# Kernel tuning notes

Measured on AMD Instinct MI355X. Metric: run time of the kernel, lower is better.

The kernel has to match this reference:

```python
import jax, jax.numpy as jnp
import numpy as np
from jax import lax

B, C, H, W, D = 2, 64, 32, 32, 32
N = H * W * D          # input_size = 32768
P = 64                 # proj_size
NH = 4                 # num_heads
HD = C // NH           # head dim = 16
LN_EPS = 1e-5
BN_EPS = 1e-5


def setup_inputs() -> dict:
    key = jax.random.key(0)
    ks = jax.random.split(key, 10)
    s = lambda k, shape: (jax.random.normal(k, shape, jnp.float32) * 0.02)
    return dict(
        x=jax.random.normal(ks[0], (B, C, H, W, D), jnp.float32),
        ln_w=jnp.ones((C,), jnp.float32), ln_b=jnp.zeros((C,), jnp.float32),
        gamma=1e-6 * jnp.ones((C,), jnp.float32),
        temp1=jnp.ones((NH, 1, 1), jnp.float32),
        temp2=jnp.ones((NH, 1, 1), jnp.float32),
        W_qkvv=s(ks[1], (4 * C, C)),                      # Linear(C,4C), no bias
        W_EF=s(ks[2], (P, N)), b_EF=jnp.zeros((P,), jnp.float32),  # shared E=F
        W_o1=s(ks[3], (C // 2, C)), b_o1=jnp.zeros((C // 2,), jnp.float32),
        W_o2=s(ks[4], (C // 2, C)), b_o2=jnp.zeros((C // 2,), jnp.float32),
        conv1_w=s(ks[5], (C, C, 3, 3, 3)),
        conv2_w=s(ks[6], (C, C, 3, 3, 3)),
        bn1_w=jnp.ones((C,), jnp.float32), bn1_b=jnp.zeros((C,), jnp.float32),
        bn2_w=jnp.ones((C,), jnp.float32), bn2_b=jnp.zeros((C,), jnp.float32),
        conv8_w=s(ks[7], (C, C, 1, 1, 1)), conv8_b=jnp.zeros((C,), jnp.float32),
    )


def _ln(x, w, b):
    mu = jnp.mean(x, axis=-1, keepdims=True)
    var = jnp.mean(jnp.square(x - mu), axis=-1, keepdims=True)
    return (x - mu) * lax.rsqrt(var + LN_EPS) * w + b


def _l2norm(x):  # F.normalize(dim=-1), eps=1e-12
    n = jnp.sqrt(jnp.sum(jnp.square(x), axis=-1, keepdims=True))
    return x / jnp.maximum(n, 1e-12)


def _bn_eval(x, w, b):  # BatchNorm3d in eval mode, running mean 0 / var 1
    scale = (w * lax.rsqrt(jnp.float32(1.0 + BN_EPS))).reshape(1, -1, 1, 1, 1)
    return x * scale + b.reshape(1, -1, 1, 1, 1)


def _conv3d(x, w, pad):
    return lax.conv_general_dilated(
        x, w, window_strides=(1, 1, 1), padding=[(pad, pad)] * 3,
        dimension_numbers=('NCDHW', 'OIDHW', 'NCDHW'))


def _lrelu(x):
    return jnp.where(x >= 0, x, 0.01 * x)


def _epa(xn, W_qkvv, W_EF, b_EF, temp1, temp2, W_o1, b_o1, W_o2, b_o2):
    b, n, c = xn.shape
    qkvv = (xn @ W_qkvv.T).reshape(b, n, 4, NH, HD).transpose(2, 0, 3, 1, 4)  # [4,B,h,N,d]
    q, k, v_ca, v_sa = [jnp.swapaxes(qkvv[i], -2, -1) for i in range(4)]      # [B,h,d,N]
    # shared linear projection E = F over the token axis N -> P
    k_proj = jnp.einsum('bhdn,pn->bhdp', k, W_EF) + b_EF
    v_proj = jnp.einsum('bhdn,pn->bhdp', v_sa, W_EF) + b_EF
    qn, kn = _l2norm(q), _l2norm(k)
    # channel attention: [B,h,d,d]
    attn_ca = jax.nn.softmax(jnp.einsum('bhdn,bhen->bhde', qn, kn) * temp1, axis=-1)
    x_ca = jnp.einsum('bhde,bhen->bhdn', attn_ca, v_ca)                       # [B,h,d,N]
    x_ca = x_ca.transpose(0, 3, 1, 2).reshape(b, n, c)
    # spatial attention with projected K/V: [B,h,N,P]
    attn_sa = jax.nn.softmax(jnp.einsum('bhdn,bhdp->bhnp', qn, k_proj) * temp2, axis=-1)
    x_sa = jnp.einsum('bhnp,bhdp->bhnd', attn_sa, v_proj)                     # [B,h,N,d]
    # faithful to original UNETR++ code: permute(0,3,1,2) then reshape(B,N,C)
    x_sa = x_sa.transpose(0, 3, 1, 2).reshape(b, n, c)
    x_sa = x_sa @ W_o1.T + b_o1
    x_ca = x_ca @ W_o2.T + b_o2
    return jnp.concatenate([x_sa, x_ca], axis=-1)


def reference(x, ln_w, ln_b, gamma, temp1, temp2, W_qkvv, W_EF, b_EF,
              W_o1, b_o1, W_o2, b_o2, conv1_w, conv2_w,
              bn1_w, bn1_b, bn2_w, bn2_b, conv8_w, conv8_b):
    b, c, h, w, d = x.shape
    xs = x.reshape(b, c, h * w * d).transpose(0, 2, 1)  # [B,N,C]
    attn = xs + gamma * _epa(_ln(xs, ln_w, ln_b), W_qkvv, W_EF, b_EF,
                             temp1, temp2, W_o1, b_o1, W_o2, b_o2)
    attn_skip = attn.reshape(b, h, w, d, c).transpose(0, 4, 1, 2, 3)  # [B,C,H,W,D]
    # UnetResBlock (stride 1, in==out -> identity residual), BN in eval mode
    out = _lrelu(_bn_eval(_conv3d(attn_skip, conv1_w, 1), bn1_w, bn1_b))
    out = _bn_eval(_conv3d(out, conv2_w, 1), bn2_w, bn2_b)
    out = _lrelu(out + attn_skip)
    # conv8: Dropout3d (off, eval) + 1x1x1 conv with bias
    y = _conv3d(out, conv8_w, 0) + conv8_b.reshape(1, -1, 1, 1, 1)
    return attn_skip + y
```

## Files before the change

kernel.cpp:

```cpp
#include <hip/hip_runtime.h>

#define NTOK 32768

typedef __attribute__((ext_vector_type(8))) short short8;
typedef __attribute__((ext_vector_type(4))) short short4_t;
typedef __attribute__((ext_vector_type(4))) float f32x4;

__device__ __forceinline__ short f2b(float f) {
    union { float f; unsigned u; } v; v.f = f;
    unsigned r = v.u + 0x7fffu + ((v.u >> 16) & 1u);
    return (short)(r >> 16);
}
__device__ __forceinline__ float b2f(short s) {
    union { float f; unsigned u; } v;
    v.u = ((unsigned)(unsigned short)s) << 16;
    return v.f;
}

__global__ void k_repack(const float* __restrict__ w1, const float* __restrict__ w2,
                         const float* __restrict__ w8, const float* __restrict__ wef,
                         const float* __restrict__ wq, const float* __restrict__ bEF,
                         short* __restrict__ wb1, short* __restrict__ wb2,
                         short* __restrict__ wb8, short* __restrict__ wefb,
                         short* __restrict__ wqb, float* __restrict__ kp,
                         float* __restrict__ vp, float* __restrict__ qd)
{
    int i = blockIdx.x * 256 + threadIdx.x;
    if (i >= 2349312) return;
    if (i >= 2347008) { qd[i - 2347008] = 0.f; return; }
    if (i >= 2338816) {
        int j = i - 2338816;
        float v = bEF[j & 63];
        kp[j] = v; vp[j] = v; return;
    }
    if (i >= 2322432) { int j = i - 2322432; wqb[j] = f2b(wq[j]); return; }
    if (i >= 225280)  { int j = i - 225280;  wefb[j] = f2b(wef[j]); return; }
    if (i >= 221184)  { int j = i - 221184;  wb8[j] = f2b(w8[j]); return; }
    int sel = i >= 110592;
    int j = sel ? i - 110592 : i;
    int tap = j >> 12;
    int r = j & 4095;
    int oc = r >> 6, ic = r & 63;
    const float* w = sel ? w2 : w1;
    short* o = sel ? wb2 : wb1;
    o[j] = f2b(w[(oc * 64 + ic) * 27 + tap]);
}

__global__ __launch_bounds__(256) void k_ln_qkvv(
    const float* __restrict__ x, const float* __restrict__ lnw,
    const float* __restrict__ lnb, const short* __restrict__ wqb,
    short* __restrict__ qkvvb)
{
    __shared__ __align__(16) short Wl[256 * 72];
    __shared__ __align__(16) short tr[256 * 72];
    __shared__ float red1[4][64], red2[4][64];
    __shared__ float mu_s[64], rs_s[64];
    short* al = tr;

    int bid = blockIdx.x;
    int b = bid >> 9;
    int n0 = (bid & 511) << 6;
    int tid = threadIdx.x;

    for (int i = tid; i < 2048; i += 256) {
        int out = i >> 3, q8 = (i & 7) * 8;
        *(short8*)&Wl[out * 72 + q8] = *(const short8*)&wqb[out * 64 + q8];
    }

    int t = tid & 63, cq = tid >> 6;
    float xr[16];
    float s1 = 0.f, s2 = 0.f;
    const float* xb = x + (((size_t)(b * 64 + cq * 16)) << 15) + n0 + t;
#pragma unroll
    for (int j = 0; j < 16; ++j) {
        float v = xb[(size_t)j << 15];
        xr[j] = v; s1 += v; s2 += v * v;
    }
    red1[cq][t] = s1; red2[cq][t] = s2;
    __syncthreads();
    if (tid < 64) {
        float a = red1[0][tid] + red1[1][tid] + red1[2][tid] + red1[3][tid];
        float q = red2[0][tid] + red2[1][tid] + red2[2][tid] + red2[3][tid];
        float mu = a * (1.f / 64.f);
        float var = q * (1.f / 64.f) - mu * mu;
        mu_s[tid] = mu;
        rs_s[tid] = rsqrtf(var + 1e-5f);
    }
    __syncthreads();
    {
        float mu = mu_s[t], rs = rs_s[t];
        short8 p0, p1;
#pragma unroll
        for (int j = 0; j < 8; ++j) {
            int c = cq * 16 + j;
            p0[j] = f2b((xr[j] - mu) * rs * lnw[c] + lnb[c]);
        }
#pragma unroll
        for (int j = 0; j < 8; ++j) {
            int c = cq * 16 + 8 + j;
            p1[j] = f2b((xr[8 + j] - mu) * rs * lnw[c] + lnb[c]);
        }
        *(short8*)&al[t * 72 + cq * 16] = p0;
        *(short8*)&al[t * 72 + cq * 16 + 8] = p1;
    }
    __syncthreads();

    int w = tid >> 6, lane = tid & 63, l15 = lane & 15, quad = lane >> 4;
    f32x4 acc[4][4];
#pragma unroll
    for (int mt = 0; mt < 4; ++mt)
#pragma unroll
        for (int nt = 0; nt < 4; ++nt) acc[mt][nt] = (f32x4){0.f, 0.f, 0.f, 0.f};
#pragma unroll
    for (int ks = 0; ks < 2; ++ks) {
        short8 af[4], bf[4];
#pragma unroll
        for (int mt = 0; mt < 4; ++mt)
            af[mt] = *(const short8*)&al[(mt * 16 + l15) * 72 + quad * 8 + ks * 32];
#pragma unroll
        for (int nt = 0; nt < 4; ++nt)
            bf[nt] = *(const short8*)&Wl[(w * 64 + nt * 16 + l15) * 72 + quad * 8 + ks * 32];
#pragma unroll
        for (int mt = 0; mt < 4; ++mt)
#pragma unroll
            for (int nt = 0; nt < 4; ++nt)
                acc[mt][nt] = __builtin_amdgcn_mfma_f32_16x16x32_bf16(af[mt], bf[nt], acc[mt][nt], 0, 0, 0);
    }
    __syncthreads();

#pragma unroll
    for (int mt = 0; mt < 4; ++mt)
#pragma unroll
        for (int nt = 0; nt < 4; ++nt) {
            int out = w * 64 + nt * 16 + l15;
            short4_t sv;
#pragma unroll
            for (int r = 0; r < 4; ++r) sv[r] = f2b(acc[mt][nt][r]);
            *(short4_t*)&tr[out * 72 + mt * 16 + quad * 4] = sv;
        }
    __syncthreads();
    for (int i = tid; i < 2048; i += 256) {
        int o = i >> 3, tq = (i & 7) * 8;
        short8 v = *(const short8*)&tr[o * 72 + tq];
        int isel = o >> 6, h = (o >> 4) & 3, d = o & 15;
        *(short8*)&qkvvb[((size_t)(((isel * 2 + b) * 4 + h) * 16 + d) << 15) + n0 + tq] = v;
    }
}

__global__ __launch_bounds__(256) void k_pq(
    const short* __restrict__ qkvvb, const short* __restrict__ wefb,
    float* __restrict__ kp, float* __restrict__ vp, float* __restrict__ qd,
    float* __restrict__ qn_acc, float* __restrict__ kn_acc)
{
    __shared__ float redb[3][64][38];
    int kc = blockIdx.x, bh = blockIdx.y;
    int tid = threadIdx.x;
    int w = tid >> 6, lane = tid & 63, l15 = lane & 15, quad = lane >> 4;
    size_t qrow = ((size_t)(bh * 16 + l15)) << 15;
    size_t krow = ((size_t)(128 + bh * 16 + l15)) << 15;
    size_t vrow = ((size_t)(384 + bh * 16 + l15)) << 15;
    int nbase = kc * 512 + w * 128 + quad * 8;
    f32x4 acck[4], accv[4], accqd, accqq, acckk;
#pragma unroll
    for (int nt = 0; nt < 4; ++nt) {
        acck[nt] = (f32x4){0.f, 0.f, 0.f, 0.f};
        accv[nt] = (f32x4){0.f, 0.f, 0.f, 0.f};
    }
    accqd = (f32x4){0.f, 0.f, 0.f, 0.f};
    accqq = (f32x4){0.f, 0.f, 0.f, 0.f};
    acckk = (f32x4){0.f, 0.f, 0.f, 0.f};
#pragma unroll
    for (int ks = 0; ks < 4; ++ks) {
        int n = nbase + ks * 32;
        short8 qf = *(const short8*)&qkvvb[qrow + n];
        short8 kf = *(const short8*)&qkvvb[krow + n];
        short8 vf = *(const short8*)&qkvvb[vrow + n];
        accqd = __builtin_amdgcn_mfma_f32_16x16x32_bf16(qf, kf, accqd, 0, 0, 0);
        accqq = __builtin_amdgcn_mfma_f32_16x16x32_bf16(qf, qf, accqq, 0, 0, 0);
        acckk = __builtin_amdgcn_mfma_f32_16x16x32_bf16(kf, kf, acckk, 0, 0, 0);
#pragma unroll
        for (int nt = 0; nt < 4; ++nt) {
            short8 wf = *(const short8*)&wefb[(((size_t)(nt * 16 + l15)) << 15) + n];
            acck[nt] = __builtin_amdgcn_mfma_f32_16x16x32_bf16(kf, wf, acck[nt], 0, 0, 0);
            accv[nt] = __builtin_amdgcn_mfma_f32_16x16x32_bf16(vf, wf, accv[nt], 0, 0, 0);
        }
    }
    int diag = (quad == (l15 >> 2));
    float qqv = diag ? accqq[l15 & 3] : 0.f;
    float kkv = diag ? acckk[l15 & 3] : 0.f;
    if (w > 0) {
        float* p = &redb[w - 1][lane][0];
#pragma unroll
        for (int nt = 0; nt < 4; ++nt)
#pragma unroll
            for (int r = 0; r < 4; ++r) { p[nt * 4 + r] = acck[nt][r]; p[16 + nt * 4 + r] = accv[nt][r]; }
#pragma unroll
        for (int r = 0; r < 4; ++r) p[32 + r] = accqd[r];
        p[36] = qqv; p[37] = kkv;
    }
    __syncthreads();
    if (w == 0) {
#pragma unroll
        for (int wv = 0; wv < 3; ++wv) {
            const float* p = &redb[wv][lane][0];
#pragma unroll
            for (int nt = 0; nt < 4; ++nt)
#pragma unroll
                for (int r = 0; r < 4; ++r) { acck[nt][r] += p[nt * 4 + r]; accv[nt][r] += p[16 + nt * 4 + r]; }
#pragma unroll
            for (int r = 0; r < 4; ++r) accqd[r] += p[32 + r];
            qqv += p[36]; kkv += p[37];
        }
        int d = quad * 4;
#pragma unroll
        for (int nt = 0; nt < 4; ++nt)
#pragma unroll
            for (int r = 0; r < 4; ++r) {
                int idx = (bh * 16 + d + r) * 64 + nt * 16 + l15;
                atomicAdd(&kp[idx], acck[nt][r]);
                atomicAdd(&vp[idx], accv[nt][r]);
            }
#pragma unroll
        for (int r = 0; r < 4; ++r)
            atomicAdd(&qd[bh * 256 + (d + r) * 16 + l15], accqd[r]);
        if (diag) {
            atomicAdd(&qn_acc[bh * 16 + l15], qqv);
            atomicAdd(&kn_acc[bh * 16 + l15], kkv);
        }
    }
}

__global__ __launch_bounds__(256) void k_attn(
    const short* __restrict__ qkvvb, const float* __restrict__ qd,
    const float* __restrict__ qn_acc, const float* __restrict__ kn_acc,
    const float* __restrict__ temp1, const float* __restrict__ kp,
    const float* __restrict__ vp, const float* __restrict__ temp2,
    short* __restrict__ xsab, short* __restrict__ xcab)
{
    __shared__ float kl[16][68];
    __shared__ float vl[16][68];
    __shared__ float alca[16][17];
    __shared__ float iqs[16], iks[16];
    __shared__ __align__(16) short Pl[4][64][72];
    __shared__ short Ol[4][64][17];
    int bh = blockIdx.y; int b = bh >> 2, h = bh & 3;
    int tid = threadIdx.x;
    for (int i = tid; i < 1024; i += 256) {
        kl[i >> 6][i & 63] = kp[bh * 1024 + i];
        vl[i >> 6][i & 63] = vp[bh * 1024 + i];
    }
    if (tid < 32) {
        int j = tid & 15;
        float v = (tid < 16) ? qn_acc[bh * 16 + j] : kn_acc[bh * 16 + j];
        float rv = 1.f / fmaxf(sqrtf(v), 1e-12f);
        if (tid < 16) iqs[j] = rv; else iks[j] = rv;
    }
    __syncthreads();
    {
        int r = tid >> 4, e = tid & 15;
        float v = qd[bh * 256 + tid] * iqs[r] * iks[e] * temp1[h];
        float mx = v;
#pragma unroll
        for (int m = 1; m < 16; m <<= 1) mx = fmaxf(mx, __shfl_xor(mx, m));
        float ex = __expf(v - mx);
        float s = ex;
#pragma unroll
        for (int m = 1; m < 16; m <<= 1) s += __shfl_xor(s, m);
        alca[r][e] = ex / s;
    }
    __syncthreads();

    int w = tid >> 6, lane = tid & 63, l15 = lane & 15, quad = lane >> 4;
    int tw = (blockIdx.x << 8) + w * 64;
    float t2 = temp2[h];
    const short8 zero8 = {0, 0, 0, 0, 0, 0, 0, 0};
    int xs = (l15 & 7) << 3;

    short8 qb[4];
    if (quad < 2) {
#pragma unroll
        for (int tnt = 0; tnt < 4; ++tnt) {
            short8 v;
#pragma unroll
            for (int j = 0; j < 8; ++j) {
                int d = quad * 8 + j;
                short qv = qkvvb[(((size_t)(bh * 16 + d)) << 15) + tw + tnt * 16 + l15];
                v[j] = f2b(b2f(qv) * iqs[d]);
            }
            qb[tnt] = v;
        }
    } else {
#pragma unroll
        for (int tnt = 0; tnt < 4; ++tnt) qb[tnt] = zero8;
    }
    short8 ka[4];
    if (quad < 2) {
#pragma unroll
        for (int pmt = 0; pmt < 4; ++pmt) {
            short8 v;
#pragma unroll
            for (int j = 0; j < 8; ++j) v[j] = f2b(kl[quad * 8 + j][pmt * 16 + l15]);
            ka[pmt] = v;
        }
    } else {
#pragma unroll
        for (int pmt = 0; pmt < 4; ++pmt) ka[pmt] = zero8;
    }

    f32x4 st[4][4];
#pragma unroll
    for (int pmt = 0; pmt < 4; ++pmt)
#pragma unroll
        for (int tnt = 0; tnt < 4; ++tnt) st[pmt][tnt] = (f32x4){0.f, 0.f, 0.f, 0.f};
#pragma unroll
    for (int pmt = 0; pmt < 4; ++pmt)
#pragma unroll
        for (int tnt = 0; tnt < 4; ++tnt)
            st[pmt][tnt] = __builtin_amdgcn_mfma_f32_16x16x32_bf16(ka[pmt], qb[tnt], st[pmt][tnt], 0, 0, 0);

#pragma unroll
    for (int tnt = 0; tnt < 4; ++tnt) {
        int tok = tnt * 16 + l15;
        float v[16];
        float mx = -1e30f;
#pragma unroll
        for (int pmt = 0; pmt < 4; ++pmt)
#pragma unroll
            for (int r = 0; r < 4; ++r) {
                float x = st[pmt][tnt][r] * t2;
                v[pmt * 4 + r] = x; mx = fmaxf(mx, x);
            }
        mx = fmaxf(mx, __shfl_xor(mx, 16));
        mx = fmaxf(mx, __shfl_xor(mx, 32));
        float s = 0.f;
#pragma unroll
        for (int i2 = 0; i2 < 16; ++i2) { v[i2] = __expf(v[i2] - mx); s += v[i2]; }
        s += __shfl_xor(s, 16);
        s += __shfl_xor(s, 32);
        float inv = 1.f / s;
#pragma unroll
        for (int pmt = 0; pmt < 4; ++pmt)
#pragma unroll
            for (int t = 0; t < 2; ++t) {
                unsigned lo = (unsigned short)f2b(v[pmt * 4 + 2 * t] * inv);
                unsigned hi = (unsigned short)f2b(v[pmt * 4 + 2 * t + 1] * inv);
                int col = (pmt * 16 + quad * 4 + 2 * t) ^ xs;
                *(unsigned*)&Pl[w][tok][col] = lo | (hi << 16);
            }
    }

    short8 vb[2];
#pragma unroll
    for (int ks = 0; ks < 2; ++ks) {
        short8 t;
#pragma unroll
        for (int j = 0; j < 8; ++j) t[j] = f2b(vl[l15][quad * 8 + ks * 32 + j]);
        vb[ks] = t;
    }
    f32x4 vo[4];
#pragma unroll
    for (int mt = 0; mt < 4; ++mt) vo[mt] = (f32x4){0.f, 0.f, 0.f, 0.f};
#pragma unroll
    for (int mt = 0; mt < 4; ++mt) {
        int tok = mt * 16 + l15;
#pragma unroll
        for (int ks = 0; ks < 2; ++ks) {
            short8 pa = *(const short8*)&Pl[w][tok][(quad * 8 + ks * 32) ^ xs];
            vo[mt] = __builtin_amdgcn_mfma_f32_16x16x32_bf16(pa, vb[ks], vo[mt], 0, 0, 0);
        }
    }

    short8 ab[4], bb;
    if (quad < 2) {
        short8 t;
#pragma unroll
        for (int j = 0; j < 8; ++j) t[j] = f2b(alca[l15][quad * 8 + j]);
        bb = t;
#pragma unroll
        for (int mt = 0; mt < 4; ++mt) {
            short8 u;
#pragma unroll
            for (int j = 0; j < 8; ++j)
                u[j] = qkvvb[(((size_t)(256 + bh * 16 + quad * 8 + j)) << 15) + tw + mt * 16 + l15];
            ab[mt] = u;
        }
    } else {
        bb = zero8;
#pragma unroll
        for (int mt = 0; mt < 4; ++mt) ab[mt] = zero8;
    }
    f32x4 ca[4];
#pragma unroll
    for (int mt = 0; mt < 4; ++mt) ca[mt] = (f32x4){0.f, 0.f, 0.f, 0.f};
#pragma unroll
    for (int mt = 0; mt < 4; ++mt)
        ca[mt] = __builtin_amdgcn_mfma_f32_16x16x32_bf16(ab[mt], bb, ca[mt], 0, 0, 0);

#pragma unroll
    for (int mt = 0; mt < 4; ++mt)
#pragma unroll
        for (int r = 0; r < 4; ++r) {
            int tok = tw + mt * 16 + quad * 4 + r;
            xcab[((size_t)(b * NTOK + tok)) * 64 + h * 16 + l15] = f2b(ca[mt][r]);
        }

#pragma unroll
    for (int mt = 0; mt < 4; ++mt)
#pragma unroll
        for (int r = 0; r < 4; ++r)
            Ol[w][mt * 16 + quad * 4 + r][l15] = f2b(vo[mt][r]);
#pragma unroll
    for (int d = 0; d < 16; ++d) {
        short vv = Ol[w][lane][d];
        xsab[(size_t)b * 2097152 + (((size_t)(d * 4 + h)) << 15) + tw + lane] = vv;
    }
}

__global__ __launch_bounds__(256) void k_epilogue(
    const float* __restrict__ x, const short* __restrict__ xsab,
    const short* __restrict__ xcab, const float* __restrict__ Wo1,
    const float* __restrict__ bo1, const float* __restrict__ Wo2,
    const float* __restrict__ bo2, const float* __restrict__ gamma,
    float* __restrict__ attn_skip, short* __restrict__ gA)
{
    __shared__ __align__(16) short Wl[64 * 72];
    __shared__ __align__(16) short trS[128 * 72];
    int tid = threadIdx.x;
    int bidx = blockIdx.x;
    int b = bidx >> 8;
    int n0 = (bidx & 255) << 7;
    for (int i = tid; i < 4096; i += 256) {
        int row = i >> 6, c = i & 63;
        float wv = (row < 32) ? Wo1[row * 64 + c] : Wo2[(row - 32) * 64 + c];
        Wl[row * 72 + c] = f2b(wv);
    }
    __syncthreads();

    int w = tid >> 6, lane = tid & 63, l15 = lane & 15, quad = lane >> 4;
    int tw = n0 + w * 32;
    const short* sa_base = xsab + (size_t)b * 2097152;
    const short* ca_base = xcab + (size_t)b * 2097152;

    f32x4 acc_sa[2][2], acc_ca[2][2];
#pragma unroll
    for (int mt = 0; mt < 2; ++mt)
#pragma unroll
        for (int nt = 0; nt < 2; ++nt) {
            acc_sa[mt][nt] = (f32x4){0.f, 0.f, 0.f, 0.f};
            acc_ca[mt][nt] = (f32x4){0.f, 0.f, 0.f, 0.f};
        }
#pragma unroll
    for (int ks = 0; ks < 2; ++ks) {
        int ko = quad * 8 + ks * 32;
        short8 b1[2], b2[2];
#pragma unroll
        for (int nt = 0; nt < 2; ++nt) {
            b1[nt] = *(const short8*)&Wl[(nt * 16 + l15) * 72 + ko];
            b2[nt] = *(const short8*)&Wl[(32 + nt * 16 + l15) * 72 + ko];
        }
#pragma unroll
        for (int mt = 0; mt < 2; ++mt) {
            int trow = tw + mt * 16 + l15;
            short8 a1 = *(const short8*)&sa_base[(size_t)trow * 64 + ko];
            short8 a2 = *(const short8*)&ca_base[(size_t)trow * 64 + ko];
#pragma unroll
            for (int nt = 0; nt < 2; ++nt) {
                acc_sa[mt][nt] = __builtin_amdgcn_mfma_f32_16x16x32_bf16(a1, b1[nt], acc_sa[mt][nt], 0, 0, 0);
                acc_ca[mt][nt] = __builtin_amdgcn_mfma_f32_16x16x32_bf16(a2, b2[nt], acc_ca[mt][nt], 0, 0, 0);
            }
        }
    }

#pragma unroll
    for (int half = 0; half < 2; ++half) {
#pragma unroll
        for (int nt = 0; nt < 2; ++nt) {
            int c = half * 32 + nt * 16 + l15;
            float g = gamma[c];
            float bias = half ? bo2[c - 32] : bo1[c];
#pragma unroll
            for (int mt = 0; mt < 2; ++mt) {
                f32x4 a = half ? acc_ca[mt][nt] : acc_sa[mt][nt];
                int tbase = tw + mt * 16 + quad * 4;
                size_t gidx = (((size_t)(b * 64 + c)) << 15) + tbase;
                f32x4 xv = *(const f32x4*)&x[gidx];
                f32x4 o;
#pragma unroll
                for (int r = 0; r < 4; ++r) {
                    float v = xv[r] + g * (a[r] + bias);
                    o[r] = v;
                    trS[(w * 32 + mt * 16 + quad * 4 + r) * 72 + c] = f2b(v);
                }
                *(f32x4*)&attn_skip[gidx] = o;
            }
        }
    }
    __syncthreads();
    for (int i = tid; i < 1024; i += 256) {
        int tok = i >> 3, cq = (i & 7) * 8;
        short8 v = *(const short8*)&trS[tok * 72 + cq];
        *(short8*)&gA[((size_t)(b * NTOK + n0 + tok)) * 64 + cq] = v;
    }
}

template <int MODE>
__global__ __launch_bounds__(256) void k_conv3m(
    const short* __restrict__ gin, const short* __restrict__ wb,
    const float* __restrict__ bnw, const float* __restrict__ bnb,
    const float* __restrict__ skip, short* __restrict__ goutS,
    const short* __restrict__ wb8, const float* __restrict__ b8,
    float* __restrict__ io)
{
    __shared__ __align__(16) short inl_s[24480];
    __shared__ __align__(16) short wl_s[15360];
    int bx = blockIdx.x;
    int bb = bx >> 8;
    int z0 = (bx >> 3) & 31;
    int y0 = (bx & 7) * 4;
    int tid = threadIdx.x;
    int lane = tid & 63, wv = tid >> 6;
    int l15 = lane & 15, quad = lane >> 4;
    int wo = tid >> 2, wq = tid & 3;

    f32x4 acc[2][4];
#pragma unroll
    for (int s = 0; s < 2; ++s)
#pragma unroll
        for (int nt = 0; nt < 4; ++nt) acc[s][nt] = (f32x4){0.f, 0.f, 0.f, 0.f};

    for (int chunk = 0; chunk < 2; ++chunk) {
        const short* wck = wb + chunk * 32 + wq * 8;
        short8 wr[3];
#pragma unroll
        for (int t = 0; t < 3; ++t)
            wr[t] = *(const short8*)&wck[(size_t)(t * 64 + wo) * 64];
        __syncthreads();
        for (int i = tid; i < 2448; i += 256) {
            int p = i >> 2, icq = i & 3;
            int xi = p % 34; int t2 = p / 34; int yi = t2 % 6; int zi = t2 / 6;
            int gz = z0 + zi - 1, gy = y0 + yi - 1, gx = xi - 1;
            short8 v = {0, 0, 0, 0, 0, 0, 0, 0};
            if ((unsigned)gz < 32u && (unsigned)gy < 32u && (unsigned)gx < 32u)
                v = *(const short8*)&gin[((size_t)(bb * NTOK + gz * 1024 + gy * 32 + gx)) * 64 + chunk * 32 + icq * 8];
            *(short8*)&inl_s[p * 40 + icq * 8] = v;
        }
#pragma unroll
        for (int t = 0; t < 3; ++t)
            *(short8*)&wl_s[(t * 64 + wo) * 40 + wq * 8] = wr[t];

#pragma unroll
        for (int kz = 0; kz < 3; ++kz)
#pragma unroll
        for (int ky = 0; ky < 3; ++ky) {
            const int sidx = kz * 3 + ky;
            __syncthreads();
            if (sidx < 8) {
#pragma unroll
                for (int t = 0; t < 3; ++t)
                    wr[t] = *(const short8*)&wck[(size_t)(((sidx + 1) * 3 + t) * 64 + wo) * 64];
            }
            const short* wcur = &wl_s[(sidx & 1) * 7680];
            int rowb = (kz * 6 + wv + ky) * 34;
#pragma unroll
            for (int kx = 0; kx < 3; ++kx) {
                short8 bf[4];
#pragma unroll
                for (int nt = 0; nt < 4; ++nt)
                    bf[nt] = *(const short8*)&wcur[(kx * 64 + nt * 16 + l15) * 40 + quad * 8];
#pragma unroll
                for (int s = 0; s < 2; ++s) {
                    short8 af = *(const short8*)&inl_s[(rowb + s * 16 + l15 + kx) * 40 + quad * 8];
#pragma unroll
                    for (int nt = 0; nt < 4; ++nt)
                        acc[s][nt] = __builtin_amdgcn_mfma_f32_16x16x32_bf16(af, bf[nt], acc[s][nt], 0, 0, 0);
                }
            }
            if (sidx < 8) {
                short* wnext = &wl_s[((sidx + 1) & 1) * 7680];
#pragma unroll
                for (int t = 0; t < 3; ++t)
                    *(short8*)&wnext[(t * 64 + wo) * 40 + wq * 8] = wr[t];
            }
        }
    }
    __syncthreads();
    float rb = rsqrtf(1.f + 1e-5f);
    if (MODE == 0) {
        short* outS = inl_s;
#pragma unroll
        for (int nt = 0; nt < 4; ++nt) {
            int oc = nt * 16 + l15;
            float sc_ = bnw[oc] * rb, sh_ = bnb[oc];
#pragma unroll
            for (int s = 0; s < 2; ++s) {
                f32x4 v = acc[s][nt];
#pragma unroll
                for (int r = 0; r < 4; ++r) {
                    int pos = wv * 32 + s * 16 + quad * 4 + r;
                    float val = v[r] * sc_ + sh_;
                    val = val >= 0.f ? val : 0.01f * val;
                    outS[pos * 72 + oc] = f2b(val);
                }
            }
        }
        __syncthreads();
        for (int i = tid; i < 1024; i += 256) {
            int p = i >> 3, cq = i & 7;
            short8 v = *(const short8*)&outS[p * 72 + cq * 8];
            int y = p >> 5, x = p & 31;
            *(short8*)&goutS[((size_t)(bb * NTOK + z0 * 1024 + (y0 + y) * 32 + x)) * 64 + cq * 8] = v;
        }
    } else {
        float* outF = (float*)inl_s;
        short* a2_s = wl_s;
        short* w8_s = wl_s + 9216;
#pragma unroll
        for (int nt = 0; nt < 4; ++nt) {
            int oc = nt * 16 + l15;
#pragma unroll
            for (int s = 0; s < 2; ++s) {
                f32x4 v = acc[s][nt];
#pragma unroll
                for (int r = 0; r < 4; ++r) {
                    int pos = wv * 32 + s * 16 + quad * 4 + r;
                    outF[oc * 132 + pos] = v[r];
                }
            }
        }
        __syncthreads();
        f32x4 skr[8];
#pragma unroll
        for (int it = 0; it < 8; ++it) {
            int i = it * 256 + tid;
            int oc = i >> 5, xq = i & 31, pos0 = xq * 4;
            f32x4 c4 = *(const f32x4*)&outF[oc * 132 + pos0];
            int y = pos0 >> 5, xx = pos0 & 31;
            size_t g = (((size_t)(bb * 64 + oc)) << 15) + ((z0 * 32 + (y0 + y)) * 32 + xx);
            f32x4 sk = *(const f32x4*)&skip[g];
            skr[it] = sk;
            float sc_ = bnw[oc] * rb, sh_ = bnb[oc];
#pragma unroll
            for (int r = 0; r < 4; ++r) {
                float val = c4[r] * sc_ + sh_ + sk[r];
                val = val >= 0.f ? val : 0.01f * val;
                a2_s[(pos0 + r) * 72 + oc] = f2b(val);
            }
        }
        for (int i = tid; i < 512; i += 256) {
            int ocw = i >> 3, cq = i & 7;
            *(short8*)&w8_s[ocw * 80 + cq * 8] = *(const short8*)&wb8[ocw * 64 + cq * 8];
        }
        __syncthreads();
        f32x4 acc2[2][4];
#pragma unroll
        for (int s = 0; s < 2; ++s)
#pragma unroll
            for (int nt = 0; nt < 4; ++nt) acc2[s][nt] = (f32x4){0.f, 0.f, 0.f, 0.f};
#pragma unroll
        for (int ks = 0; ks < 2; ++ks) {
            short8 a8[2], b8f[4];
#pragma unroll
            for (int s = 0; s < 2; ++s)
                a8[s] = *(const short8*)&a2_s[(wv * 32 + s * 16 + l15) * 72 + quad * 8 + ks * 32];
#pragma unroll
            for (int nt = 0; nt < 4; ++nt)
                b8f[nt] = *(const short8*)&w8_s[(nt * 16 + l15) * 80 + quad * 8 + ks * 32];
#pragma unroll
            for (int s = 0; s < 2; ++s)
#pragma unroll
                for (int nt = 0; nt < 4; ++nt)
                    acc2[s][nt] = __builtin_amdgcn_mfma_f32_16x16x32_bf16(a8[s], b8f[nt], acc2[s][nt], 0, 0, 0);
        }
        __syncthreads();
#pragma unroll
        for (int nt = 0; nt < 4; ++nt) {
            int oc = nt * 16 + l15;
#pragma unroll
            for (int s = 0; s < 2; ++s) {
                f32x4 v = acc2[s][nt];
#pragma unroll
                for (int r = 0; r < 4; ++r) {
                    int pos = wv * 32 + s * 16 + quad * 4 + r;
                    outF[oc * 132 + pos] = v[r];
                }
            }
        }
        __syncthreads();
#pragma unroll
        for (int it = 0; it < 8; ++it) {
            int i = it * 256 + tid;
            int oc = i >> 5, xq = i & 31, pos0 = xq * 4;
            f32x4 cv = *(const f32x4*)&outF[oc * 132 + pos0];
            int y = pos0 >> 5, xx = pos0 & 31;
            size_t g = (((size_t)(bb * 64 + oc)) << 15) + ((z0 * 32 + (y0 + y)) * 32 + xx);
            float bias8 = b8[oc];
            f32x4 o;
#pragma unroll
            for (int r = 0; r < 4; ++r) o[r] = skr[it][r] + cv[r] + bias8;
            *(f32x4*)&io[g] = o;
        }
    }
}

extern "C" void kernel_launch(void* const* d_in, const int* in_sizes, int n_in,
                              void* d_out, int out_size, void* d_ws, size_t ws_size,
                              hipStream_t stream) {
    const float* x      = (const float*)d_in[0];
    const float* ln_w   = (const float*)d_in[1];
    const float* ln_b   = (const float*)d_in[2];
    const float* gamma  = (const float*)d_in[3];
    const float* temp1  = (const float*)d_in[4];
    const float* temp2  = (const float*)d_in[5];
    const float* W_qkvv = (const float*)d_in[6];
    const float* W_EF   = (const float*)d_in[7];
    const float* b_EF   = (const float*)d_in[8];
    const float* W_o1   = (const float*)d_in[9];
    const float* b_o1   = (const float*)d_in[10];
    const float* W_o2   = (const float*)d_in[11];
    const float* b_o2   = (const float*)d_in[12];
    const float* conv1w = (const float*)d_in[13];
    const float* conv2w = (const float*)d_in[14];
    const float* bn1_w  = (const float*)d_in[15];
    const float* bn1_b  = (const float*)d_in[16];
    const float* bn2_w  = (const float*)d_in[17];
    const float* bn2_b  = (const float*)d_in[18];
    const float* conv8w = (const float*)d_in[19];
    const float* conv8b = (const float*)d_in[20];

    short* qkvvb = (short*)d_ws;
    float* kp    = (float*)(qkvvb + 16777216);
    float* vp    = kp + 8192;
    float* qd    = vp + 8192;
    float* qn_acc= qd + 2048;
    float* kn_acc= qn_acc + 128;
    float* a_ca  = kn_acc + 128;
    float* iqn   = a_ca + 2048;
    float* ikn   = iqn + 128;
    short* xcab  = (short*)(ikn + 128);
    short* xsab  = xcab + 4194304;
    short* gA    = xsab + 4194304;
    short* g1    = gA + 4194304;
    short* wb1   = g1 + 4194304;
    short* wb2   = wb1 + 110592;
    short* wb8   = wb2 + 110592;
    short* wefb  = wb8 + 4096;
    short* wqb   = wefb + 2097152;

    float* attn_skip = (float*)d_out;

    hipLaunchKernelGGL(k_repack, dim3(9177), dim3(256), 0, stream,
                       conv1w, conv2w, conv8w, W_EF, W_qkvv, b_EF,
                       wb1, wb2, wb8, wefb, wqb, kp, vp, qd);
    hipLaunchKernelGGL(k_ln_qkvv, dim3(1024), dim3(256), 0, stream,
                       x, ln_w, ln_b, wqb, qkvvb);
    hipLaunchKernelGGL(k_pq, dim3(64, 8), dim3(256), 0, stream,
                       qkvvb, wefb, kp, vp, qd, qn_acc, kn_acc);
    hipLaunchKernelGGL(k_attn, dim3(128, 8), dim3(256), 0, stream,
                       qkvvb, qd, qn_acc, kn_acc, temp1, kp, vp, temp2, xsab, xcab);
    hipLaunchKernelGGL(k_epilogue, dim3(512), dim3(256), 0, stream,
                       x, xsab, xcab, W_o1, b_o1, W_o2, b_o2, gamma, attn_skip, gA);
    hipLaunchKernelGGL((k_conv3m<0>), dim3(512), dim3(256), 0, stream,
                       gA, wb1, bn1_w, bn1_b, (const float*)nullptr, g1,
                       (const short*)nullptr, (const float*)nullptr, (float*)nullptr);
    hipLaunchKernelGGL((k_conv3m<1>), dim3(512), dim3(256), 0, stream,
                       g1, wb2, bn2_w, bn2_b, attn_skip, (short*)nullptr,
                       wb8, conv8b, attn_skip);
}
```

Measured before the change: 218.0 us.

## Read conv activations directly from global memory with smaller tiles and more blocks

The 3D conv kernels stop staging the input halo tile in LDS. MFMA A-fragments are now loaded straight from global memory (relying on the cache), and whole kz/ky taps that fall outside the volume are skipped. The per-block tile shrinks from 4 rows to 2 rows, and the 4 waves are split across y-row and output-channel halves. This cuts LDS to about 30KB so more blocks fit per CU, with launch_bounds set to 4 blocks. The MODE 1 epilogue also drops its fp32 LDS transpose round-trips and works on registers, at the cost of uncoalesced strided global loads and repeated input reads.

Result: slower. 287.0 us (+31.7%).

```diff
diff --git a/kernel.cpp b/kernel.cpp
--- a/kernel.cpp
+++ b/kernel.cpp
@@ -504,29 +504,31 @@
 }
 
 template <int MODE>
-__global__ __launch_bounds__(256) void k_conv3m(
+__global__ __launch_bounds__(256, 4) void k_conv3m(
     const short* __restrict__ gin, const short* __restrict__ wb,
     const float* __restrict__ bnw, const float* __restrict__ bnb,
     const float* __restrict__ skip, short* __restrict__ goutS,
     const short* __restrict__ wb8, const float* __restrict__ b8,
     float* __restrict__ io)
 {
-    __shared__ __align__(16) short inl_s[24480];
-    __shared__ __align__(16) short wl_s[15360];
+    __shared__ __align__(16) short ls[15360];
     int bx = blockIdx.x;
-    int bb = bx >> 8;
-    int z0 = (bx >> 3) & 31;
-    int y0 = (bx & 7) * 4;
+    int bb = bx >> 9;
+    int z0 = (bx >> 4) & 31;
+    int y0 = (bx & 15) * 2;
     int tid = threadIdx.x;
     int lane = tid & 63, wv = tid >> 6;
     int l15 = lane & 15, quad = lane >> 4;
     int wo = tid >> 2, wq = tid & 3;
-
-    f32x4 acc[2][4];
+    int yw = wv >> 1;
+    int och = wv & 1;
+    const short8 zero8 = {0, 0, 0, 0, 0, 0, 0, 0};
+
+    f32x4 acc[2][2];
 #pragma unroll
     for (int s = 0; s < 2; ++s)
 #pragma unroll
-        for (int nt = 0; nt < 4; ++nt) acc[s][nt] = (f32x4){0.f, 0.f, 0.f, 0.f};
+        for (int nt = 0; nt < 2; ++nt) acc[s][nt] = (f32x4){0.f, 0.f, 0.f, 0.f};
 
     for (int chunk = 0; chunk < 2; ++chunk) {
         const short* wck = wb + chunk * 32 + wq * 8;
@@ -535,18 +537,9 @@
         for (int t = 0; t < 3; ++t)
             wr[t] = *(const short8*)&wck[(size_t)(t * 64 + wo) * 64];
         __syncthreads();
-        for (int i = tid; i < 2448; i += 256) {
-            int p = i >> 2, icq = i & 3;
-            int xi = p % 34; int t2 = p / 34; int yi = t2 % 6; int zi = t2 / 6;
-            int gz = z0 + zi - 1, gy = y0 + yi - 1, gx = xi - 1;
-            short8 v = {0, 0, 0, 0, 0, 0, 0, 0};
-            if ((unsigned)gz < 32u && (unsigned)gy < 32u && (unsigned)gx < 32u)
-                v = *(const short8*)&gin[((size_t)(bb * NTOK + gz * 1024 + gy * 32 + gx)) * 64 + chunk * 32 + icq * 8];
-            *(short8*)&inl_s[p * 40 + icq * 8] = v;
-        }
 #pragma unroll
         for (int t = 0; t < 3; ++t)
-            *(short8*)&wl_s[(t * 64 + wo) * 40 + wq * 8] = wr[t];
+            *(short8*)&ls[(t * 64 + wo) * 40 + wq * 8] = wr[t];
 
 #pragma unroll
         for (int kz = 0; kz < 3; ++kz)
@@ -559,24 +552,28 @@
                 for (int t = 0; t < 3; ++t)
                     wr[t] = *(const short8*)&wck[(size_t)(((sidx + 1) * 3 + t) * 64 + wo) * 64];
             }
-            const short* wcur = &wl_s[(sidx & 1) * 7680];
-            int rowb = (kz * 6 + wv + ky) * 34;
-#pragma unroll
-            for (int kx = 0; kx < 3; ++kx) {
-                short8 bf[4];
-#pragma unroll
-                for (int nt = 0; nt < 4; ++nt)
-                    bf[nt] = *(const short8*)&wcur[(kx * 64 + nt * 16 + l15) * 40 + quad * 8];
-#pragma unroll
-                for (int s = 0; s < 2; ++s) {
-                    short8 af = *(const short8*)&inl_s[(rowb + s * 16 + l15 + kx) * 40 + quad * 8];
-#pragma unroll
-                    for (int nt = 0; nt < 4; ++nt)
-                        acc[s][nt] = __builtin_amdgcn_mfma_f32_16x16x32_bf16(af, bf[nt], acc[s][nt], 0, 0, 0);
+            const short* wcur = &ls[(sidx & 1) * 7680];
+            int gz = z0 + kz - 1;
+            int gy = y0 + yw + ky - 1;
+            if (((unsigned)gz < 32u) & ((unsigned)gy < 32u)) {
+                size_t rowbase = ((size_t)(bb * NTOK + gz * 1024 + gy * 32)) * 64 + chunk * 32 + quad * 8;
+#pragma unroll
+                for (int kx = 0; kx < 3; ++kx) {
+                    short8 bf0 = *(const short8*)&wcur[(kx * 64 + och * 32 + l15) * 40 + quad * 8];
+                    short8 bf1 = *(const short8*)&wcur[(kx * 64 + och * 32 + 16 + l15) * 40 + quad * 8];
+#pragma unroll
+                    for (int s = 0; s < 2; ++s) {
+                        int gx = s * 16 + l15 + kx - 1;
+                        short8 af = zero8;
+                        if ((unsigned)gx < 32u)
+                            af = *(const short8*)&gin[rowbase + (size_t)gx * 64];
+                        acc[s][0] = __builtin_amdgcn_mfma_f32_16x16x32_bf16(af, bf0, acc[s][0], 0, 0, 0);
+                        acc[s][1] = __builtin_amdgcn_mfma_f32_16x16x32_bf16(af, bf1, acc[s][1], 0, 0, 0);
+                    }
                 }
             }
             if (sidx < 8) {
-                short* wnext = &wl_s[((sidx + 1) & 1) * 7680];
+                short* wnext = &ls[((sidx + 1) & 1) * 7680];
 #pragma unroll
                 for (int t = 0; t < 3; ++t)
                     *(short8*)&wnext[(t * 64 + wo) * 40 + wq * 8] = wr[t];
@@ -586,17 +583,17 @@
     __syncthreads();
     float rb = rsqrtf(1.f + 1e-5f);
     if (MODE == 0) {
-        short* outS = inl_s;
-#pragma unroll
-        for (int nt = 0; nt < 4; ++nt) {
-            int oc = nt * 16 + l15;
+        short* outS = ls;
+#pragma unroll
+        for (int nt = 0; nt < 2; ++nt) {
+            int oc = och * 32 + nt * 16 + l15;
             float sc_ = bnw[oc] * rb, sh_ = bnb[oc];
 #pragma unroll
             for (int s = 0; s < 2; ++s) {
                 f32x4 v = acc[s][nt];
 #pragma unroll
                 for (int r = 0; r < 4; ++r) {
-                    int pos = wv * 32 + s * 16 + quad * 4 + r;
+                    int pos = yw * 32 + s * 16 + quad * 4 + r;
                     float val = v[r] * sc_ + sh_;
                     val = val >= 0.f ? val : 0.01f * val;
                     outS[pos * 72 + oc] = f2b(val);
@@ -604,46 +601,34 @@
             }
         }
         __syncthreads();
-        for (int i = tid; i < 1024; i += 256) {
+        for (int i = tid; i < 512; i += 256) {
             int p = i >> 3, cq = i & 7;
             short8 v = *(const short8*)&outS[p * 72 + cq * 8];
             int y = p >> 5, x = p & 31;
             *(short8*)&goutS[((size_t)(bb * NTOK + z0 * 1024 + (y0 + y) * 32 + x)) * 64 + cq * 8] = v;
         }
     } else {
-        float* outF = (float*)inl_s;
-        short* a2_s = wl_s;
-        short* w8_s = wl_s + 9216;
-#pragma unroll
-        for (int nt = 0; nt < 4; ++nt) {
-            int oc = nt * 16 + l15;
+        short* a2_s = ls;
+        short* w8_s = ls + 4608;
+        f32x4 skr[2][2];
+#pragma unroll
+        for (int nt = 0; nt < 2; ++nt) {
+            int oc = och * 32 + nt * 16 + l15;
+            float sc_ = bnw[oc] * rb, sh_ = bnb[oc];
 #pragma unroll
             for (int s = 0; s < 2; ++s) {
+                size_t g = (((size_t)(bb * 64 + oc)) << 15) +
+                           ((z0 * 32 + y0 + yw) * 32 + s * 16 + quad * 4);
+                f32x4 sk = *(const f32x4*)&skip[g];
+                skr[s][nt] = sk;
                 f32x4 v = acc[s][nt];
 #pragma unroll
                 for (int r = 0; r < 4; ++r) {
-                    int pos = wv * 32 + s * 16 + quad * 4 + r;
-                    outF[oc * 132 + pos] = v[r];
+                    int pos = yw * 32 + s * 16 + quad * 4 + r;
+                    float val = v[r] * sc_ + sh_ + sk[r];
+                    val = val >= 0.f ? val : 0.01f * val;
+                    a2_s[pos * 72 + oc] = f2b(val);
                 }
-            }
-        }
-        __syncthreads();
-        f32x4 skr[8];
-#pragma unroll
-        for (int it = 0; it < 8; ++it) {
-            int i = it * 256 + tid;
-            int oc = i >> 5, xq = i & 31, pos0 = xq * 4;
-            f32x4 c4 = *(const f32x4*)&outF[oc * 132 + pos0];
-            int y = pos0 >> 5, xx = pos0 & 31;
-            size_t g = (((size_t)(bb * 64 + oc)) << 15) + ((z0 * 32 + (y0 + y)) * 32 + xx);
-            f32x4 sk = *(const f32x4*)&skip[g];
-            skr[it] = sk;
-            float sc_ = bnw[oc] * rb, sh_ = bnb[oc];
-#pragma unroll
-            for (int r = 0; r < 4; ++r) {
-                float val = c4[r] * sc_ + sh_ + sk[r];
-                val = val >= 0.f ? val : 0.01f * val;
-                a2_s[(pos0 + r) * 72 + oc] = f2b(val);
             }
         }
         for (int i = tid; i < 512; i += 256) {
@@ -651,53 +636,39 @@
             *(short8*)&w8_s[ocw * 80 + cq * 8] = *(const short8*)&wb8[ocw * 64 + cq * 8];
         }
         __syncthreads();
-        f32x4 acc2[2][4];
+        f32x4 acc2[2][2];
 #pragma unroll
         for (int s = 0; s < 2; ++s)
 #pragma unroll
-            for (int nt = 0; nt < 4; ++nt) acc2[s][nt] = (f32x4){0.f, 0.f, 0.f, 0.f};
+            for (int nt = 0; nt < 2; ++nt) acc2[s][nt] = (f32x4){0.f, 0.f, 0.f, 0.f};
 #pragma unroll
         for (int ks = 0; ks < 2; ++ks) {
-            short8 a8[2], b8f[4];
+            short8 a8[2], b8f[2];
 #pragma unroll
             for (int s = 0; s < 2; ++s)
-                a8[s] = *(const short8*)&a2_s[(wv * 32 + s * 16 + l15) * 72 + quad * 8 + ks * 32];
-#pragma unroll
-            for (int nt = 0; nt < 4; ++nt)
-                b8f[nt] = *(const short8*)&w8_s[(nt * 16 + l15) * 80 + quad * 8 + ks * 32];
+                a8[s] = *(const short8*)&a2_s[(yw * 32 + s * 16 + l15) * 72 + quad * 8 + ks * 32];
+#pragma unroll
+            for (int nt = 0; nt < 2; ++nt)
+                b8f[nt] = *(const short8*)&w8_s[(och * 32 + nt * 16 + l15) * 80 + quad * 8 + ks * 32];
 #pragma unroll
             for (int s = 0; s < 2; ++s)
 #pragma unroll
-                for (int nt = 0; nt < 4; ++nt)
+                for (int nt = 0; nt < 2; ++nt)
                     acc2[s][nt] = __builtin_amdgcn_mfma_f32_16x16x32_bf16(a8[s], b8f[nt], acc2[s][nt], 0, 0, 0);
         }
-        __syncthreads();
-#pragma unroll
-        for (int nt = 0; nt < 4; ++nt) {
-            int oc = nt * 16 + l15;
+#pragma unroll
+        for (int nt = 0; nt < 2; ++nt) {
+            int oc = och * 32 + nt * 16 + l15;
+            float bias8 = b8[oc];
 #pragma unroll
             for (int s = 0; s < 2; ++s) {
-                f32x4 v = acc2[s][nt];
-#pragma unroll
-                for (int r = 0; r < 4; ++r) {
-                    int pos = wv * 32 + s * 16 + quad * 4 + r;
-                    outF[oc * 132 + pos] = v[r];
-                }
-            }
-        }
-        __syncthreads();
-#pragma unroll
-        for (int it = 0; it < 8; ++it) {
-            int i = it * 256 + tid;
-            int oc = i >> 5, xq = i & 31, pos0 = xq * 4;
-            f32x4 cv = *(const f32x4*)&outF[oc * 132 + pos0];
-            int y = pos0 >> 5, xx = pos0 & 31;
-            size_t g = (((size_t)(bb * 64 + oc)) << 15) + ((z0 * 32 + (y0 + y)) * 32 + xx);
-            float bias8 = b8[oc];
-            f32x4 o;
-#pragma unroll
-            for (int r = 0; r < 4; ++r) o[r] = skr[it][r] + cv[r] + bias8;
-            *(f32x4*)&io[g] = o;
+                size_t g = (((size_t)(bb * 64 + oc)) << 15) +
+                           ((z0 * 32 + y0 + yw) * 32 + s * 16 + quad * 4);
+                f32x4 o;
+#pragma unroll
+                for (int r = 0; r < 4; ++r) o[r] = skr[s][nt][r] + acc2[s][nt][r] + bias8;
+                *(f32x4*)&io[g] = o;
+            }
         }
     }
 }
@@ -759,10 +730,10 @@
                        qkvvb, qd, qn_acc, kn_acc, temp1, kp, vp, temp2, xsab, xcab);
     hipLaunchKernelGGL(k_epilogue, dim3(512), dim3(256), 0, stream,
                        x, xsab, xcab, W_o1, b_o1, W_o2, b_o2, gamma, attn_skip, gA);
-    hipLaunchKernelGGL((k_conv3m<0>), dim3(512), dim3(256), 0, stream,
+    hipLaunchKernelGGL((k_conv3m<0>), dim3(1024), dim3(256), 0, stream,
                        gA, wb1, bn1_w, bn1_b, (const float*)nullptr, g1,
                        (const short*)nullptr, (const float*)nullptr, (float*)nullptr);
-    hipLaunchKernelGGL((k_conv3m<1>), dim3(512), dim3(256), 0, stream,
+    hipLaunchKernelGGL((k_conv3m<1>), dim3(1024), dim3(256), 0, stream,
                        g1, wb2, bn2_w, bn2_b, attn_skip, (short*)nullptr,
                        wb8, conv8b, attn_skip);
 }
```
